# Kernel tuning notes

Measured on AMD Instinct MI355X. Metric: run time of the kernel, lower is better.

The kernel has to match this reference:

```python
import jax, jax.numpy as jnp
import numpy as np

B, T, C = 1024, 512, 48

def setup_inputs() -> dict:
    key = jax.random.key(0)
    k1, k2, k3 = jax.random.split(key, 3)
    potentials = jax.random.normal(k1, (B, T, C), dtype=jnp.float32)
    sequence_lengths = jax.random.randint(k2, (B, 1), 1, T).astype(jnp.int32)
    # layer weight: uniform initializer (keras default uniform is U[-0.05, 0.05])
    transitions = jax.random.uniform(k3, (C, C), dtype=jnp.float32, minval=-0.05, maxval=0.05)
    return {"potentials": potentials, "sequence_lengths": sequence_lengths, "transitions": transitions}

def reference(potentials, sequence_lengths, transitions):
    # Faithful jax port of tf.contrib.crf.crf_decode (Viterbi max-plus DP),
    # followed by one_hot as in CRFLayer.call (inference branch of in_train_phase).
    Bb, Tt, Cc = potentials.shape
    seq_len = sequence_lengths.reshape(-1)  # K.flatten

    def fwd_step(score, xs):
        # score: [B,C] viterbi scores at step t-1
        pot_t, t = xs
        total = score[:, :, None] + transitions[None]  # [B, C_prev, C_cur]
        bp = jnp.argmax(total, axis=1).astype(jnp.int32)  # [B,C] best prev tag
        new_score = jnp.max(total, axis=1) + pot_t        # [B,C]
        valid = (t < seq_len)[:, None]                    # mask steps past seq_len
        score = jnp.where(valid, new_score, score)
        bp = jnp.where(valid, bp, jnp.arange(Cc, dtype=jnp.int32)[None])
        return score, bp

    init = potentials[:, 0]                               # [B,C]
    xs = (jnp.swapaxes(potentials[:, 1:], 0, 1), jnp.arange(1, Tt))
    last_score, bps = jax.lax.scan(fwd_step, init, xs)    # bps: [T-1,B,C]

    last_tag = jnp.argmax(last_score, axis=-1).astype(jnp.int32)  # [B]

    def back_step(tag_next, bp):
        prev = jnp.take_along_axis(bp, tag_next[:, None], axis=1)[:, 0]
        return prev, tag_next

    first_tag, tags_rest = jax.lax.scan(back_step, last_tag, bps, reverse=True)
    tags = jnp.concatenate([first_tag[None], tags_rest], axis=0)  # [T,B]
    tags = jnp.swapaxes(tags, 0, 1)                               # [B,T]
    return jax.nn.one_hot(tags, Cc, dtype=potentials.dtype)       # [B,T,C]
```

## Files before the change

### kernel.cpp

```cpp
#include <hip/hip_runtime.h>

#define T_DIM 512
#define C_DIM 48
#define BPS   64
#define CH    4

typedef float f32x2 __attribute__((ext_vector_type(2)));
typedef float f32x4 __attribute__((ext_vector_type(4)));

#if __has_builtin(__builtin_amdgcn_readlane)
#define READLANE_I(v, l) __builtin_amdgcn_readlane((v), (l))
#else
#define READLANE_I(v, l) __shfl((v), (l), 64)
#endif

#if __has_builtin(__builtin_amdgcn_wave_barrier)
#define WAVE_SYNC() do { __asm__ __volatile__("" ::: "memory"); __builtin_amdgcn_wave_barrier(); } while (0)
#else
#define WAVE_SYNC() __asm__ __volatile__("" ::: "memory")
#endif

__device__ __forceinline__ unsigned umin_(unsigned a, unsigned b) { return a < b ? a : b; }

#define MAX3(a, b, c) fmaxf(fmaxf((a), (b)), (c))
#define CV(I_)  (cv2[(I_) / 2][(I_) & 1])
#define UU(I_)  (__float_as_uint(d2[(I_) / 2][(I_) & 1]) | (unsigned)(I_))
#define EMIN3(I_) umin_(umin_(UU(I_), UU((I_) + 1)), UU((I_) + 2))

#define VSTEP(T_, PV_) do {                                                  \
    const int nsi_ = __float_as_int(ns);                                     \
    float su_[C_DIM];                                                        \
    _Pragma("unroll")                                                        \
    for (int k_ = 0; k_ < C_DIM; ++k_)                                       \
        su_[k_] = __int_as_float(READLANE_I(nsi_, k_));                      \
    f32x2 cv2[24];                                                           \
    _Pragma("unroll")                                                        \
    for (int m_ = 0; m_ < 24; ++m_) {                                        \
        cv2[m_][0] = su_[2 * m_]     + tc2[m_][0];                           \
        cv2[m_][1] = su_[2 * m_ + 1] + tc2[m_][1];                           \
    }                                                                        \
    float A0  = MAX3(CV(0),  CV(1),  CV(2));                                 \
    float A1  = MAX3(CV(3),  CV(4),  CV(5));                                 \
    float A2  = MAX3(CV(6),  CV(7),  CV(8));                                 \
    float A3  = MAX3(CV(9),  CV(10), CV(11));                                \
    float A4  = MAX3(CV(12), CV(13), CV(14));                                \
    float A5  = MAX3(CV(15), CV(16), CV(17));                                \
    float A6  = MAX3(CV(18), CV(19), CV(20));                                \
    float A7  = MAX3(CV(21), CV(22), CV(23));                                \
    float A8  = MAX3(CV(24), CV(25), CV(26));                                \
    float A9  = MAX3(CV(27), CV(28), CV(29));                                \
    float A10 = MAX3(CV(30), CV(31), CV(32));                                \
    float A11 = MAX3(CV(33), CV(34), CV(35));                                \
    float A12 = MAX3(CV(36), CV(37), CV(38));                                \
    float A13 = MAX3(CV(39), CV(40), CV(41));                                \
    float A14 = MAX3(CV(42), CV(43), CV(44));                                \
    float A15 = MAX3(CV(45), CV(46), CV(47));                                \
    float B0 = MAX3(A0,  A1,  A2);                                           \
    float B1 = MAX3(A3,  A4,  A5);                                           \
    float B2 = MAX3(A6,  A7,  A8);                                           \
    float B3 = MAX3(A9,  A10, A11);                                          \
    float B4 = MAX3(A12, A13, A14);                                          \
    float Cx0 = MAX3(B0, B1, B2);                                            \
    float Cx1 = MAX3(B3, B4, A15);                                           \
    const float m_v = fmaxf(Cx0, Cx1);                                       \
    f32x2 d2[24];                                                            \
    _Pragma("unroll")                                                        \
    for (int k_ = 0; k_ < 24; ++k_) d2[k_] = cv2[k_] - m_v;      \
    unsigned U0  = EMIN3(0);   unsigned U1  = EMIN3(3);                      \
    unsigned U2  = EMIN3(6);   unsigned U3  = EMIN3(9);                      \
    unsigned U4  = EMIN3(12);  unsigned U5  = EMIN3(15);                     \
    unsigned U6  = EMIN3(18);  unsigned U7  = EMIN3(21);                     \
    unsigned U8  = EMIN3(24);  unsigned U9  = EMIN3(27);                     \
    unsigned U10 = EMIN3(30);  unsigned U11 = EMIN3(33);                     \
    unsigned U12 = EMIN3(36);  unsigned U13 = EMIN3(39);                     \
    unsigned U14 = EMIN3(42);  unsigned U15 = EMIN3(45);                     \
    unsigned V0 = umin_(umin_(U0,  U1),  U2);                                \
    unsigned V1 = umin_(umin_(U3,  U4),  U5);                                \
    unsigned V2 = umin_(umin_(U6,  U7),  U8);                                \
    unsigned V3 = umin_(umin_(U9,  U10), U11);                               \
    unsigned V4 = umin_(umin_(U12, U13), U14);                               \
    unsigned W0 = umin_(umin_(V0, V1), V2);                                  \
    unsigned W1 = umin_(umin_(V3, V4), U15);                                 \
    const unsigned wi_ = umin_(W0, W1);                                      \
    ns = m_v + (PV_);                                                        \
    bp[(T_) * BPS + tid] = (unsigned char)wi_;     \
} while (0)

__global__ __launch_bounds__(64) void crf_viterbi(
    const float* __restrict__ pot,
    const int*   __restrict__ seqlen,
    const float* __restrict__ trans,
    float*       __restrict__ out)
{
    const int b   = blockIdx.x;
    const int tid = threadIdx.x;
    const int jj  = (tid < C_DIM) ? tid : (C_DIM - 1);

    __shared__ unsigned char bp[T_DIM * BPS];
    __shared__ __align__(4) unsigned char tags[T_DIM];
    __shared__ __align__(16) float fsc[64];

    const float* potb = pot + (size_t)b * (T_DIM * C_DIM);
    const int L   = seqlen[b];
    const int thi = L - 1;

    f32x2 tc2[24];
#pragma unroll
    for (int k = 0; k < 24; ++k) {
        tc2[k][0] = trans[(2 * k)     * C_DIM + jj];
        tc2[k][1] = trans[(2 * k + 1) * C_DIM + jj];
    }

    float ns = potb[jj];

    const float* pp = potb + jj;

    float pb[CH];
#pragma unroll
    for (int k = 0; k < CH; ++k) {
        int tt = 1 + k; if (tt > T_DIM - 1) tt = T_DIM - 1;
        pb[k] = pp[tt * C_DIM];
    }
    for (int t0 = 1; t0 < L; t0 += CH) {
        float nb[CH];
#pragma unroll
        for (int k = 0; k < CH; ++k) {
            int tt = t0 + CH + k; if (tt > T_DIM - 1) tt = T_DIM - 1;
            nb[k] = pp[tt * C_DIM];
        }
#pragma unroll
        for (int k = 0; k < CH; ++k) {
            const int t = t0 + k;
            if (t >= L) break;
            VSTEP(t, pb[k]);
        }
#pragma unroll
        for (int k = 0; k < CH; ++k) pb[k] = nb[k];
    }

    fsc[tid] = ns;
    WAVE_SYNC();
    __syncthreads();

    const float* fs = fsc;
    float bv = fs[0];
    int   bi = 0;
#pragma unroll
    for (int i = 1; i < C_DIM; ++i) {
        float v = fs[i];
        if (v > bv) { bv = v; bi = i; }
    }
    const int last_tag = __builtin_amdgcn_readfirstlane(bi);

    for (int t = L + tid; t < T_DIM; t += 64) tags[t] = (unsigned char)last_tag;

    int y = last_tag;
    for (int c0 = (thi >> 6) << 6; c0 >= 0; c0 -= 64) {
        int row[64];
#pragma unroll
        for (int k = 0; k < 64; ++k) row[k] = bp[(c0 + k) * BPS + jj];

        int vacc = 0;
#pragma unroll
        for (int k = 63; k >= 0; --k) {
            const int t = c0 + k;
            vacc = (tid == k) ? y : vacc;
            const int ynew = READLANE_I(row[k], y);
            if ((unsigned)(t - 1) < (unsigned)thi) y = ynew;
        }
        const int tk = c0 + tid;
        if (tk <= thi) tags[tk] = (unsigned char)(vacc & 0xff);
    }
    __syncthreads();

    if (tid < C_DIM) {
        const int r = tid / 12;
        const int q = tid - r * 12;
        const int cbase = q * 4;
        float* ob = out + (size_t)b * (T_DIM * C_DIM);
        for (int t0 = 0; t0 < T_DIM; t0 += 4) {
            const unsigned int tg4 = *(const unsigned int*)&tags[t0];
            const int mytag = (int)((tg4 >> (r * 8)) & 0xffu);
            float4 v;
            v.x = (cbase + 0 == mytag) ? 1.0f : 0.0f;
            v.y = (cbase + 1 == mytag) ? 1.0f : 0.0f;
            v.z = (cbase + 2 == mytag) ? 1.0f : 0.0f;
            v.w = (cbase + 3 == mytag) ? 1.0f : 0.0f;
            *(float4*)(ob + (size_t)(t0 + r) * C_DIM + cbase) = v;
        }
    }
}

extern "C" void kernel_launch(void* const* d_in, const int* in_sizes, int n_in,
                              void* d_out, int out_size, void* d_ws, size_t ws_size,
                              hipStream_t stream) {
    const float* pot    = (const float*)d_in[0];
    const int*   sl     = (const int*)d_in[1];
    const float* trans  = (const float*)d_in[2];
    float*       out    = (float*)d_out;
    const int B = in_sizes[1];
    crf_viterbi<<<B, 64, 0, stream>>>(pot, sl, trans, out);
}
```

Measured before the change: 360.0 us.

## Prune Viterbi predecessor candidates with a transition-bound threshold via wave ballot

Replaces the dense 48-way max/argmax over all previous tags with a sparse scan. A lane bound derived from the maximum absolute transition value selects, through a wave ballot, only the previous tags whose score could still win. Transitions are staged in LDS, and per-step potential maxima come from DPP wave reductions. This removes most of the readlane and max/min work per step. In exchange each step pays a serial ballot/ctz/readlane/LDS loop whose length depends on the data. Backpointer stride also shrinks to 48, so lanes 48–63 spill into the next row.

Result: faster. 289.4 us (-19.6%).

```diff
diff --git a/kernel.cpp b/kernel.cpp
--- a/kernel.cpp
+++ b/kernel.cpp
@@ -2,11 +2,8 @@
 
 #define T_DIM 512
 #define C_DIM 48
-#define BPS   64
+#define BPS   48
 #define CH    4
-
-typedef float f32x2 __attribute__((ext_vector_type(2)));
-typedef float f32x4 __attribute__((ext_vector_type(4)));
 
 #if __has_builtin(__builtin_amdgcn_readlane)
 #define READLANE_I(v, l) __builtin_amdgcn_readlane((v), (l))
@@ -20,71 +17,22 @@
 #define WAVE_SYNC() __asm__ __volatile__("" ::: "memory")
 #endif
 
-__device__ __forceinline__ unsigned umin_(unsigned a, unsigned b) { return a < b ? a : b; }
+#define DPP_MAX_STEP(V_, CTRL_) do {                                          \
+    int o_ = __builtin_amdgcn_update_dpp(__float_as_int(V_),                  \
+                                         __float_as_int(V_),                  \
+                                         (CTRL_), 0xF, 0xF, false);           \
+    V_ = fmaxf(V_, __int_as_float(o_));                                       \
+} while (0)
 
-#define MAX3(a, b, c) fmaxf(fmaxf((a), (b)), (c))
-#define CV(I_)  (cv2[(I_) / 2][(I_) & 1])
-#define UU(I_)  (__float_as_uint(d2[(I_) / 2][(I_) & 1]) | (unsigned)(I_))
-#define EMIN3(I_) umin_(umin_(UU(I_), UU((I_) + 1)), UU((I_) + 2))
-
-#define VSTEP(T_, PV_) do {                                                  \
-    const int nsi_ = __float_as_int(ns);                                     \
-    float su_[C_DIM];                                                        \
-    _Pragma("unroll")                                                        \
-    for (int k_ = 0; k_ < C_DIM; ++k_)                                       \
-        su_[k_] = __int_as_float(READLANE_I(nsi_, k_));                      \
-    f32x2 cv2[24];                                                           \
-    _Pragma("unroll")                                                        \
-    for (int m_ = 0; m_ < 24; ++m_) {                                        \
-        cv2[m_][0] = su_[2 * m_]     + tc2[m_][0];                           \
-        cv2[m_][1] = su_[2 * m_ + 1] + tc2[m_][1];                           \
-    }                                                                        \
-    float A0  = MAX3(CV(0),  CV(1),  CV(2));                                 \
-    float A1  = MAX3(CV(3),  CV(4),  CV(5));                                 \
-    float A2  = MAX3(CV(6),  CV(7),  CV(8));                                 \
-    float A3  = MAX3(CV(9),  CV(10), CV(11));                                \
-    float A4  = MAX3(CV(12), CV(13), CV(14));                                \
-    float A5  = MAX3(CV(15), CV(16), CV(17));                                \
-    float A6  = MAX3(CV(18), CV(19), CV(20));                                \
-    float A7  = MAX3(CV(21), CV(22), CV(23));                                \
-    float A8  = MAX3(CV(24), CV(25), CV(26));                                \
-    float A9  = MAX3(CV(27), CV(28), CV(29));                                \
-    float A10 = MAX3(CV(30), CV(31), CV(32));                                \
-    float A11 = MAX3(CV(33), CV(34), CV(35));                                \
-    float A12 = MAX3(CV(36), CV(37), CV(38));                                \
-    float A13 = MAX3(CV(39), CV(40), CV(41));                                \
-    float A14 = MAX3(CV(42), CV(43), CV(44));                                \
-    float A15 = MAX3(CV(45), CV(46), CV(47));                                \
-    float B0 = MAX3(A0,  A1,  A2);                                           \
-    float B1 = MAX3(A3,  A4,  A5);                                           \
-    float B2 = MAX3(A6,  A7,  A8);                                           \
-    float B3 = MAX3(A9,  A10, A11);                                          \
-    float B4 = MAX3(A12, A13, A14);                                          \
-    float Cx0 = MAX3(B0, B1, B2);                                            \
-    float Cx1 = MAX3(B3, B4, A15);                                           \
-    const float m_v = fmaxf(Cx0, Cx1);                                       \
-    f32x2 d2[24];                                                            \
-    _Pragma("unroll")                                                        \
-    for (int k_ = 0; k_ < 24; ++k_) d2[k_] = cv2[k_] - m_v;      \
-    unsigned U0  = EMIN3(0);   unsigned U1  = EMIN3(3);                      \
-    unsigned U2  = EMIN3(6);   unsigned U3  = EMIN3(9);                      \
-    unsigned U4  = EMIN3(12);  unsigned U5  = EMIN3(15);                     \
-    unsigned U6  = EMIN3(18);  unsigned U7  = EMIN3(21);                     \
-    unsigned U8  = EMIN3(24);  unsigned U9  = EMIN3(27);                     \
-    unsigned U10 = EMIN3(30);  unsigned U11 = EMIN3(33);                     \
-    unsigned U12 = EMIN3(36);  unsigned U13 = EMIN3(39);                     \
-    unsigned U14 = EMIN3(42);  unsigned U15 = EMIN3(45);                     \
-    unsigned V0 = umin_(umin_(U0,  U1),  U2);                                \
-    unsigned V1 = umin_(umin_(U3,  U4),  U5);                                \
-    unsigned V2 = umin_(umin_(U6,  U7),  U8);                                \
-    unsigned V3 = umin_(umin_(U9,  U10), U11);                               \
-    unsigned V4 = umin_(umin_(U12, U13), U14);                               \
-    unsigned W0 = umin_(umin_(V0, V1), V2);                                  \
-    unsigned W1 = umin_(umin_(V3, V4), U15);                                 \
-    const unsigned wi_ = umin_(W0, W1);                                      \
-    ns = m_v + (PV_);                                                        \
-    bp[(T_) * BPS + tid] = (unsigned char)wi_;     \
-} while (0)
+__device__ __forceinline__ float wave_max_f(float v) {
+    DPP_MAX_STEP(v, 0x111);
+    DPP_MAX_STEP(v, 0x112);
+    DPP_MAX_STEP(v, 0x114);
+    DPP_MAX_STEP(v, 0x118);
+    DPP_MAX_STEP(v, 0x142);
+    DPP_MAX_STEP(v, 0x143);
+    return __int_as_float(READLANE_I(__float_as_int(v), 63));
+}
 
 __global__ __launch_bounds__(64) void crf_viterbi(
     const float* __restrict__ pot,
@@ -96,6 +44,7 @@
     const int tid = threadIdx.x;
     const int jj  = (tid < C_DIM) ? tid : (C_DIM - 1);
 
+    __shared__ __align__(16) float trl[C_DIM * C_DIM];
     __shared__ unsigned char bp[T_DIM * BPS];
     __shared__ __align__(4) unsigned char tags[T_DIM];
     __shared__ __align__(16) float fsc[64];
@@ -104,23 +53,32 @@
     const int L   = seqlen[b];
     const int thi = L - 1;
 
-    f32x2 tc2[24];
-#pragma unroll
-    for (int k = 0; k < 24; ++k) {
-        tc2[k][0] = trans[(2 * k)     * C_DIM + jj];
-        tc2[k][1] = trans[(2 * k + 1) * C_DIM + jj];
+    float tm = 0.0f;
+    for (int i = tid; i < C_DIM * C_DIM; i += 64) {
+        float v = trans[i];
+        trl[i] = v;
+        tm = fmaxf(tm, fabsf(v));
     }
+    const float tmax = wave_max_f(tm);
+    const float nC5 = -(5.0f * tmax + 1e-3f);
+    const float nC2 = -(2.0f * tmax + 1e-3f);
+    WAVE_SYNC();
 
     float ns = potb[jj];
+    float vthr = wave_max_f(ns) + nC2;
 
     const float* pp = potb + jj;
 
     float pb[CH];
+    float pmr[CH];
 #pragma unroll
     for (int k = 0; k < CH; ++k) {
         int tt = 1 + k; if (tt > T_DIM - 1) tt = T_DIM - 1;
         pb[k] = pp[tt * C_DIM];
     }
+#pragma unroll
+    for (int k = 0; k < CH; ++k) pmr[k] = wave_max_f(pb[k]);
+
     for (int t0 = 1; t0 < L; t0 += CH) {
         float nb[CH];
 #pragma unroll
@@ -132,10 +90,30 @@
         for (int k = 0; k < CH; ++k) {
             const int t = t0 + k;
             if (t >= L) break;
-            VSTEP(t, pb[k]);
+            unsigned long long mm =
+                __ballot(ns >= vthr) & 0x0000FFFFFFFFFFFFull;
+            if (!mm) mm = 0x0000FFFFFFFFFFFFull;
+            int c = (int)__builtin_ctzll(mm); mm &= mm - 1;
+            float s_c = __int_as_float(READLANE_I(__float_as_int(ns), c));
+            float m  = s_c + trl[c * C_DIM + jj];
+            int   wi = c;
+            while (mm) {
+                int c2 = (int)__builtin_ctzll(mm); mm &= mm - 1;
+                float s2 = __int_as_float(READLANE_I(__float_as_int(ns), c2));
+                float cv = s2 + trl[c2 * C_DIM + jj];
+                bool g = cv > m;
+                m  = g ? cv : m;
+                wi = g ? c2 : wi;
+            }
+            bp[t * BPS + tid] = (unsigned char)wi;
+            ns   = m + pb[k];
+            vthr = (m + pmr[k]) + nC5;
         }
+        float pmn[CH];
 #pragma unroll
-        for (int k = 0; k < CH; ++k) pb[k] = nb[k];
+        for (int k = 0; k < CH; ++k) pmn[k] = wave_max_f(nb[k]);
+#pragma unroll
+        for (int k = 0; k < CH; ++k) { pb[k] = nb[k]; pmr[k] = pmn[k]; }
     }
 
     fsc[tid] = ns;
```
